# Optimization experiments

Hardware: AMD Instinct MI355X
Metric: run time of the kernel (lower is better)

The kernel has to match this reference:

```python
import jax, jax.numpy as jnp
from jax import lax
import numpy as np

NB_HEAD = 8
D_MODEL = 64
KERNEL = 3


def setup_inputs() -> dict:
    key = jax.random.key(0)
    k1, k2, k3, k4, k5 = jax.random.split(key, 5)
    B, N, T, D = 16, 1024, 24, D_MODEL
    value = jax.random.normal(k1, (B, N, T, D), dtype=jnp.float32)
    # Conv2d(d_model, d_model, (1, kernel_size)) weights (OIHW) + bias
    fan_in = D * 1 * KERNEL
    bound = 1.0 / np.sqrt(fan_in)
    W_conv = jax.random.uniform(k2, (D, D, 1, KERNEL), jnp.float32, -bound, bound)
    b_conv = jax.random.uniform(k3, (D,), jnp.float32, -bound, bound)
    # Linear(d_model, d_model): W (out, in), bias (out,)
    lb = 1.0 / np.sqrt(D)
    W_lin = jax.random.uniform(k4, (D, D), jnp.float32, -lb, lb)
    b_lin = jax.random.uniform(k5, (D,), jnp.float32, -lb, lb)
    return {"value": value, "W_conv": W_conv, "b_conv": b_conv,
            "W_lin": W_lin, "b_lin": b_lin}


def reference(value, W_conv, b_conv, W_lin, b_lin):
    B, N, T, D = value.shape
    h = NB_HEAD
    d_k = D // h
    pad = (KERNEL - 1) // 2
    # conv1D_aware_temporal_context1 on value.permute(0,3,1,2): (B, D, N, T)
    x = jnp.transpose(value, (0, 3, 1, 2))
    x = lax.conv_general_dilated(
        x, W_conv, window_strides=(1, 1), padding=[(0, 0), (pad, pad)],
        dimension_numbers=("NCHW", "OIHW", "NCHW"))
    x = x + b_conv[None, :, None, None]
    # view(B, h, d_k, N, T).permute(0,3,1,4,2) -> (B, N, h, T, d_k)
    v = jnp.transpose(x.reshape(B, h, d_k, N, T), (0, 3, 1, 4, 2))
    # relation_matrix_h is the tridiagonal all-ones band -> out[t] = v[t-1]+v[t]+v[t+1]
    vp = jnp.pad(v, ((0, 0), (0, 0), (0, 0), (1, 1), (0, 0)))
    v = vp[..., :-2, :] + vp[..., 1:-1, :] + vp[..., 2:, :]
    # transpose(2,3) then merge heads: (B, N, T, h*d_k)
    v = jnp.transpose(v, (0, 1, 3, 2, 4)).reshape(B, N, T, h * d_k)
    # linear_output1 + relu
    out = jax.nn.relu(jnp.einsum("bntd,od->bnto", v, W_lin) + b_lin)
    return out
```

## Files before the change

kernel.cpp:

```cpp
#include <hip/hip_runtime.h>
#include <hip/hip_bf16.h>


typedef __attribute__((ext_vector_type(8))) short short8;
typedef __attribute__((ext_vector_type(8))) __bf16 bf16x8;
typedef __attribute__((ext_vector_type(4))) float f4;

#define R_ROWS 8
#define VP_STRIDE 72
#define V_ROW_ELEMS (26 * VP_STRIDE)

__device__ __forceinline__ unsigned short f2bfu(float f) {
    return __bfloat16_as_ushort(__float2bfloat16(f));
}

__global__ void prep_kernel(const float* __restrict__ Wconv,
                            const float* __restrict__ bconv,
                            const float* __restrict__ Wlin,
                            const float* __restrict__ blin,
                            __hip_bfloat16* __restrict__ wbig,
                            float* __restrict__ biasC,
                            float* __restrict__ blinF) {
    __shared__ float Wl[4096];
    const int tid = threadIdx.x;
    for (int c = tid; c < 4096; c += 256) Wl[c] = Wlin[c];
    __syncthreads();
    int idx = blockIdx.x * 256 + tid;
    if (idx < 64 * 192) {
        int o = idx / 192;
        int j = idx - o * 192;
        int k = j >> 6;
        int i = j & 63;
        float acc = 0.0f;
        for (int c = 0; c < 64; ++c)
            acc += Wl[o * 64 + c] * Wconv[c * 192 + i * 3 + k];
        wbig[o * 192 + j] = __float2bfloat16(acc);
    } else if (idx < 64 * 192 + 64) {
        int o = idx - 64 * 192;
        float acc = 0.0f;
        for (int c = 0; c < 64; ++c)
            acc += Wl[o * 64 + c] * bconv[c];
        biasC[o] = acc;
    } else if (idx < 64 * 192 + 128) {
        int o = idx - (64 * 192 + 64);
        blinF[o] = blin[o];
    }
}

__global__ __launch_bounds__(256, 4) void fused_kernel(
    const float* __restrict__ value,
    const __hip_bfloat16* __restrict__ wbig,
    const float* __restrict__ biasC,
    const float* __restrict__ blinF,
    float* __restrict__ out) {
    __shared__ __align__(16) short Vlds[R_ROWS * V_ROW_ELEMS];

    const int tid = threadIdx.x;
    const int wave = tid >> 6;
    const int lane = tid & 63;
    const int lane15 = lane & 15;
    const int quad = lane >> 4;
    const long base_row = (long)blockIdx.x * R_ROWS;

    for (int c4 = tid; c4 < 3072; c4 += 256) {
        int r = c4 / 384;
        int rem = c4 - r * 384;
        int t = rem >> 4;
        int d4 = (rem & 15) << 2;
        f4 v = *(const f4*)(value + (base_row + r) * 1536 + t * 64 + d4);
        ushort4 u;
        u.x = f2bfu(v.x); u.y = f2bfu(v.y); u.z = f2bfu(v.z); u.w = f2bfu(v.w);
        *(ushort4*)(Vlds + r * V_ROW_ELEMS + (t + 1) * VP_STRIDE + d4) = u;
    }
    if (tid < 128) {
        int r = tid >> 4;
        int which = (tid >> 3) & 1;
        int d8 = (tid & 7) << 3;
        uint4 z; z.x = 0; z.y = 0; z.z = 0; z.w = 0;
        *(uint4*)(Vlds + r * V_ROW_ELEMS + which * (25 * VP_STRIDE) + d8) = z;
    }
    __syncthreads();

    f4 acc[3][4];
    #pragma unroll
    for (int a = 0; a < 3; ++a)
        #pragma unroll
        for (int b = 0; b < 4; ++b) {
            f4 zz = {0.f, 0.f, 0.f, 0.f};
            acc[a][b] = zz;
        }

    const int mt0 = wave * 3;
    int aoff[3];
    #pragma unroll
    for (int mt = 0; mt < 3; ++mt) {
        int m = (mt0 + mt) * 16 + lane15;
        int r = m / 24;
        int s = m - r * 24;
        aoff[mt] = r * V_ROW_ELEMS + s * VP_STRIDE;
    }
    const short* wsrc = (const short*)wbig;
    const int k0 = quad * 8;
    #pragma unroll
    for (int ks = 0; ks < 6; ++ks) {
        int k = ks * 32 + k0;
        int ka = ((k >> 6) * VP_STRIDE) + (k & 63);
        bf16x8 bfr[4], afr[3];
        #pragma unroll
        for (int nt = 0; nt < 4; ++nt)
            bfr[nt] = __builtin_bit_cast(bf16x8,
                *(const short8*)(wsrc + (nt * 16 + lane15) * 192 + k));
        #pragma unroll
        for (int mt = 0; mt < 3; ++mt)
            afr[mt] = __builtin_bit_cast(bf16x8,
                *(const short8*)(Vlds + aoff[mt] + ka));
        #pragma unroll
        for (int mt = 0; mt < 3; ++mt)
            #pragma unroll
            for (int nt = 0; nt < 4; ++nt)
                acc[mt][nt] = __builtin_amdgcn_mfma_f32_16x16x32_bf16(
                    afr[mt], bfr[nt], acc[mt][nt], 0, 0, 0);
    }

    float b3[4], b2[4];
    #pragma unroll
    for (int nt = 0; nt < 4; ++nt) {
        int o = nt * 16 + lane15;
        float bc = biasC[o];
        float bl = blinF[o];
        b3[nt] = 3.0f * bc + bl;
        b2[nt] = 2.0f * bc + bl;
    }
    const int srcP = (lane + 48) & 63;
    const int srcN = (lane + 16) & 63;
    #pragma unroll
    for (int mt = 0; mt < 3; ++mt) {
        const int mtp = (mt > 0) ? mt - 1 : 0;
        const int mtn = (mt < 2) ? mt + 1 : 2;
        #pragma unroll
        for (int nt = 0; nt < 4; ++nt) {
            float pin = __shfl(acc[mt][nt][3], srcP, 64);
            float pxr = __shfl(acc[mtp][nt][3], srcP, 64);
            float nin = __shfl(acc[mt][nt][0], srcN, 64);
            float nxr = __shfl(acc[mtn][nt][0], srcN, 64);
            float prev0 = (quad == 0) ? pxr : pin;
            float next3 = (quad == 3) ? nxr : nin;
            #pragma unroll
            for (int i = 0; i < 4; ++i) {
                int tq = mt * 16 + quad * 4 + i;
                int rr = (tq >= 24) ? 1 : 0;
                int t = tq - rr * 24;
                float s = acc[mt][nt][i];
                float prev = (i > 0) ? acc[mt][nt][i - 1] : prev0;
                float next = (i < 3) ? acc[mt][nt][i + 1] : next3;
                if (t > 0)  s += prev;
                if (t < 23) s += next;
                float bias = (t == 0 || t == 23) ? b2[nt] : b3[nt];
                float r = fmaxf(s + bias, 0.0f);
                long addr = ((base_row + 2 * wave + rr) * 24 + t) * 64
                            + nt * 16 + lane15;
                out[addr] = r;
            }
        }
    }
}

extern "C" void kernel_launch(void* const* d_in, const int* in_sizes, int n_in,
                              void* d_out, int out_size, void* d_ws, size_t ws_size,
                              hipStream_t stream) {
    const float* value = (const float*)d_in[0];
    const float* Wconv = (const float*)d_in[1];
    const float* bconv = (const float*)d_in[2];
    const float* Wlin  = (const float*)d_in[3];
    const float* blin  = (const float*)d_in[4];
    float* out = (float*)d_out;

    __hip_bfloat16* wbig = (__hip_bfloat16*)d_ws;
    float* biasC = (float*)((char*)d_ws + 24576);
    float* blinF = (float*)((char*)d_ws + 24832);

    prep_kernel<<<49, 256, 0, stream>>>(Wconv, bconv, Wlin, blin, wbig, biasC, blinF);
    fused_kernel<<<2048, 256, 0, stream>>>(value, wbig, biasC, blinF, out);
}
```

Baseline: 209.1 us.

## Persist blocks over four row groups with double-buffered LDS prefetch

Each block now processes four 8-row groups instead of one. The next group's global loads are issued into registers before the current group's MFMA work, then written to a second LDS buffer afterwards. Work is also split so each wave owns one 16-column output slice across all 12 M tiles, with its weight fragments held in registers for the whole kernel. The aim is to overlap memory loads with compute and cut repeated weight loads and block launch overhead. In exchange it doubles LDS use, raises register pressure, lowers occupancy (launch bounds 4 to 2), and launches only 512 blocks.

```diff
diff --git a/kernel.cpp b/kernel.cpp
--- a/kernel.cpp
+++ b/kernel.cpp
@@ -7,6 +7,7 @@
 typedef __attribute__((ext_vector_type(4))) float f4;
 
 #define R_ROWS 8
+#define GROUPS 4
 #define VP_STRIDE 72
 #define V_ROW_ELEMS (26 * VP_STRIDE)
 
@@ -47,121 +48,149 @@
     }
 }
 
-__global__ __launch_bounds__(256, 4) void fused_kernel(
+__global__ __launch_bounds__(256, 2) void fused_kernel(
     const float* __restrict__ value,
     const __hip_bfloat16* __restrict__ wbig,
     const float* __restrict__ biasC,
     const float* __restrict__ blinF,
     float* __restrict__ out) {
-    __shared__ __align__(16) short Vlds[R_ROWS * V_ROW_ELEMS];
+    __shared__ __align__(16) short Vlds[2][R_ROWS * V_ROW_ELEMS];
 
     const int tid = threadIdx.x;
     const int wave = tid >> 6;
     const int lane = tid & 63;
     const int lane15 = lane & 15;
     const int quad = lane >> 4;
-    const long base_row = (long)blockIdx.x * R_ROWS;
-
-    for (int c4 = tid; c4 < 3072; c4 += 256) {
+    const long block_row0 = (long)blockIdx.x * (R_ROWS * GROUPS);
+
+    int goff[12], loff[12];
+    #pragma unroll
+    for (int j = 0; j < 12; ++j) {
+        int c4 = tid + 256 * j;
         int r = c4 / 384;
         int rem = c4 - r * 384;
         int t = rem >> 4;
         int d4 = (rem & 15) << 2;
-        f4 v = *(const f4*)(value + (base_row + r) * 1536 + t * 64 + d4);
-        ushort4 u;
-        u.x = f2bfu(v.x); u.y = f2bfu(v.y); u.z = f2bfu(v.z); u.w = f2bfu(v.w);
-        *(ushort4*)(Vlds + r * V_ROW_ELEMS + (t + 1) * VP_STRIDE + d4) = u;
+        goff[j] = r * 1536 + t * 64 + d4;
+        loff[j] = r * V_ROW_ELEMS + (t + 1) * VP_STRIDE + d4;
     }
     if (tid < 128) {
         int r = tid >> 4;
         int which = (tid >> 3) & 1;
         int d8 = (tid & 7) << 3;
         uint4 z; z.x = 0; z.y = 0; z.z = 0; z.w = 0;
-        *(uint4*)(Vlds + r * V_ROW_ELEMS + which * (25 * VP_STRIDE) + d8) = z;
+        *(uint4*)(&Vlds[0][0] + r * V_ROW_ELEMS + which * (25 * VP_STRIDE) + d8) = z;
+        *(uint4*)(&Vlds[1][0] + r * V_ROW_ELEMS + which * (25 * VP_STRIDE) + d8) = z;
+    }
+
+    const short* wsrc = (const short*)wbig;
+    const int k0 = quad * 8;
+    bf16x8 breg[6];
+    #pragma unroll
+    for (int ks = 0; ks < 6; ++ks)
+        breg[ks] = __builtin_bit_cast(bf16x8,
+            *(const short8*)(wsrc + (wave * 16 + lane15) * 192 + ks * 32 + k0));
+
+    f4 pre[12];
+    {
+        const float* vb = value + block_row0 * 1536;
+        #pragma unroll
+        for (int j = 0; j < 12; ++j)
+            pre[j] = *(const f4*)(vb + goff[j]);
+        #pragma unroll
+        for (int j = 0; j < 12; ++j) {
+            ushort4 u;
+            u.x = f2bfu(pre[j].x); u.y = f2bfu(pre[j].y);
+            u.z = f2bfu(pre[j].z); u.w = f2bfu(pre[j].w);
+            *(ushort4*)(&Vlds[0][0] + loff[j]) = u;
+        }
     }
     __syncthreads();
 
-    f4 acc[3][4];
+    int aoff[12];
     #pragma unroll
-    for (int a = 0; a < 3; ++a)
-        #pragma unroll
-        for (int b = 0; b < 4; ++b) {
-            f4 zz = {0.f, 0.f, 0.f, 0.f};
-            acc[a][b] = zz;
-        }
-
-    const int mt0 = wave * 3;
-    int aoff[3];
-    #pragma unroll
-    for (int mt = 0; mt < 3; ++mt) {
-        int m = (mt0 + mt) * 16 + lane15;
+    for (int mt = 0; mt < 12; ++mt) {
+        int m = mt * 16 + lane15;
         int r = m / 24;
         int s = m - r * 24;
         aoff[mt] = r * V_ROW_ELEMS + s * VP_STRIDE;
     }
-    const short* wsrc = (const short*)wbig;
-    const int k0 = quad * 8;
-    #pragma unroll
-    for (int ks = 0; ks < 6; ++ks) {
-        int k = ks * 32 + k0;
-        int ka = ((k >> 6) * VP_STRIDE) + (k & 63);
-        bf16x8 bfr[4], afr[3];
-        #pragma unroll
-        for (int nt = 0; nt < 4; ++nt)
-            bfr[nt] = __builtin_bit_cast(bf16x8,
-                *(const short8*)(wsrc + (nt * 16 + lane15) * 192 + k));
-        #pragma unroll
-        for (int mt = 0; mt < 3; ++mt)
-            afr[mt] = __builtin_bit_cast(bf16x8,
-                *(const short8*)(Vlds + aoff[mt] + ka));
-        #pragma unroll
-        for (int mt = 0; mt < 3; ++mt)
-            #pragma unroll
-            for (int nt = 0; nt < 4; ++nt)
-                acc[mt][nt] = __builtin_amdgcn_mfma_f32_16x16x32_bf16(
-                    afr[mt], bfr[nt], acc[mt][nt], 0, 0, 0);
-    }
-
-    float b3[4], b2[4];
-    #pragma unroll
-    for (int nt = 0; nt < 4; ++nt) {
-        int o = nt * 16 + lane15;
-        float bc = biasC[o];
-        float bl = blinF[o];
-        b3[nt] = 3.0f * bc + bl;
-        b2[nt] = 2.0f * bc + bl;
-    }
+
+    const int o = wave * 16 + lane15;
+    const float bc = biasC[o];
+    const float bl = blinF[o];
+    const float b3 = 3.0f * bc + bl;
+    const float b2 = 2.0f * bc + bl;
     const int srcP = (lane + 48) & 63;
     const int srcN = (lane + 16) & 63;
-    #pragma unroll
-    for (int mt = 0; mt < 3; ++mt) {
-        const int mtp = (mt > 0) ? mt - 1 : 0;
-        const int mtn = (mt < 2) ? mt + 1 : 2;
-        #pragma unroll
-        for (int nt = 0; nt < 4; ++nt) {
-            float pin = __shfl(acc[mt][nt][3], srcP, 64);
-            float pxr = __shfl(acc[mtp][nt][3], srcP, 64);
-            float nin = __shfl(acc[mt][nt][0], srcN, 64);
-            float nxr = __shfl(acc[mtn][nt][0], srcN, 64);
+
+    int p = 0;
+    for (int g = 0; g < GROUPS; ++g) {
+        if (g + 1 < GROUPS) {
+            const float* vb = value + (block_row0 + (long)(g + 1) * R_ROWS) * 1536;
+            #pragma unroll
+            for (int j = 0; j < 12; ++j)
+                pre[j] = *(const f4*)(vb + goff[j]);
+        }
+
+        const short* Vcur = &Vlds[p][0];
+        f4 acc[12];
+        #pragma unroll
+        for (int mt = 0; mt < 12; ++mt) {
+            f4 zz = {0.f, 0.f, 0.f, 0.f};
+            acc[mt] = zz;
+        }
+        #pragma unroll
+        for (int ks = 0; ks < 6; ++ks) {
+            int k = ks * 32 + k0;
+            int ka = ((k >> 6) * VP_STRIDE) + (k & 63);
+            #pragma unroll
+            for (int mt = 0; mt < 12; ++mt) {
+                bf16x8 a = __builtin_bit_cast(bf16x8,
+                    *(const short8*)(Vcur + aoff[mt] + ka));
+                acc[mt] = __builtin_amdgcn_mfma_f32_16x16x32_bf16(
+                    a, breg[ks], acc[mt], 0, 0, 0);
+            }
+        }
+
+        const long grow0 = block_row0 + (long)g * R_ROWS;
+        #pragma unroll
+        for (int mt = 0; mt < 12; ++mt) {
+            const int mtp = (mt > 0) ? mt - 1 : 0;
+            const int mtn = (mt < 11) ? mt + 1 : 11;
+            float pin = __shfl(acc[mt][3], srcP, 64);
+            float pxr = __shfl(acc[mtp][3], srcP, 64);
+            float nin = __shfl(acc[mt][0], srcN, 64);
+            float nxr = __shfl(acc[mtn][0], srcN, 64);
             float prev0 = (quad == 0) ? pxr : pin;
             float next3 = (quad == 3) ? nxr : nin;
             #pragma unroll
             for (int i = 0; i < 4; ++i) {
-                int tq = mt * 16 + quad * 4 + i;
-                int rr = (tq >= 24) ? 1 : 0;
-                int t = tq - rr * 24;
-                float s = acc[mt][nt][i];
-                float prev = (i > 0) ? acc[mt][nt][i - 1] : prev0;
-                float next = (i < 3) ? acc[mt][nt][i + 1] : next3;
+                int rowq = mt * 16 + quad * 4 + i;
+                int rr = rowq / 24;
+                int t = rowq - rr * 24;
+                float s = acc[mt][i];
+                float prev = (i > 0) ? acc[mt][i - 1] : prev0;
+                float next = (i < 3) ? acc[mt][i + 1] : next3;
                 if (t > 0)  s += prev;
                 if (t < 23) s += next;
-                float bias = (t == 0 || t == 23) ? b2[nt] : b3[nt];
-                float r = fmaxf(s + bias, 0.0f);
-                long addr = ((base_row + 2 * wave + rr) * 24 + t) * 64
-                            + nt * 16 + lane15;
-                out[addr] = r;
+                float r = fmaxf(s + ((t == 0 || t == 23) ? b2 : b3), 0.0f);
+                out[((grow0 + rr) * 24 + t) * 64 + o] = r;
             }
         }
+
+        if (g + 1 < GROUPS) {
+            short* Vnxt = &Vlds[p ^ 1][0];
+            #pragma unroll
+            for (int j = 0; j < 12; ++j) {
+                ushort4 u;
+                u.x = f2bfu(pre[j].x); u.y = f2bfu(pre[j].y);
+                u.z = f2bfu(pre[j].z); u.w = f2bfu(pre[j].w);
+                *(ushort4*)(Vnxt + loff[j]) = u;
+            }
+            __syncthreads();
+        }
+        p ^= 1;
     }
 }
 
@@ -180,5 +209,5 @@
     float* blinF = (float*)((char*)d_ws + 24832);
 
     prep_kernel<<<49, 256, 0, stream>>>(Wconv, bconv, Wlin, blin, wbig, biasC, blinF);
-    fused_kernel<<<2048, 256, 0, stream>>>(value, wbig, biasC, blinF, out);
-}
+    fused_kernel<<<512, 256, 0, stream>>>(value, wbig, biasC, blinF, out);
+}
```

Result: faster. 200.1 us (-4.3%).

## Drop LDS staging; load value directly into MFMA B-fragments per wave row

Applied to the files above, without the earlier changes.

Each wave now handles one (b,n) row and reads its fp32 activations straight from global memory into bf16 MFMA operands, replacing the LDS staging buffer and the block-wide barrier. The GEMM is transposed so weights form the A operand and time steps the columns, with 2 time tiles padded to 32 (8 wasted lanes). The temporal neighbour sum uses ds_bpermute within quads, and the grid doubles to 4096 blocks. This removes LDS traffic and synchronisation, at the cost of redundant overlapping global loads (each value row is reread for three time shifts) and padded MFMA work.

```diff
diff --git a/kernel.cpp b/kernel.cpp
--- a/kernel.cpp
+++ b/kernel.cpp
@@ -5,14 +5,6 @@
 typedef __attribute__((ext_vector_type(8))) short short8;
 typedef __attribute__((ext_vector_type(8))) __bf16 bf16x8;
 typedef __attribute__((ext_vector_type(4))) float f4;
-
-#define R_ROWS 8
-#define VP_STRIDE 72
-#define V_ROW_ELEMS (26 * VP_STRIDE)
-
-__device__ __forceinline__ unsigned short f2bfu(float f) {
-    return __bfloat16_as_ushort(__float2bfloat16(f));
-}
 
 __global__ void prep_kernel(const float* __restrict__ Wconv,
                             const float* __restrict__ bconv,
@@ -47,119 +39,103 @@
     }
 }
 
+__device__ __forceinline__ float bperm(int idx, float v) {
+    return __int_as_float(__builtin_amdgcn_ds_bpermute(idx, __float_as_int(v)));
+}
+
 __global__ __launch_bounds__(256, 4) void fused_kernel(
     const float* __restrict__ value,
     const __hip_bfloat16* __restrict__ wbig,
     const float* __restrict__ biasC,
     const float* __restrict__ blinF,
     float* __restrict__ out) {
-    __shared__ __align__(16) short Vlds[R_ROWS * V_ROW_ELEMS];
-
     const int tid = threadIdx.x;
-    const int wave = tid >> 6;
     const int lane = tid & 63;
     const int lane15 = lane & 15;
     const int quad = lane >> 4;
-    const long base_row = (long)blockIdx.x * R_ROWS;
+    const long row = (long)blockIdx.x * 4 + (tid >> 6);
+    const float* vrow = value + row * 1536;
 
-    for (int c4 = tid; c4 < 3072; c4 += 256) {
-        int r = c4 / 384;
-        int rem = c4 - r * 384;
-        int t = rem >> 4;
-        int d4 = (rem & 15) << 2;
-        f4 v = *(const f4*)(value + (base_row + r) * 1536 + t * 64 + d4);
-        ushort4 u;
-        u.x = f2bfu(v.x); u.y = f2bfu(v.y); u.z = f2bfu(v.z); u.w = f2bfu(v.w);
-        *(ushort4*)(Vlds + r * V_ROW_ELEMS + (t + 1) * VP_STRIDE + d4) = u;
-    }
-    if (tid < 128) {
-        int r = tid >> 4;
-        int which = (tid >> 3) & 1;
-        int d8 = (tid & 7) << 3;
-        uint4 z; z.x = 0; z.y = 0; z.z = 0; z.w = 0;
-        *(uint4*)(Vlds + r * V_ROW_ELEMS + which * (25 * VP_STRIDE) + d8) = z;
-    }
-    __syncthreads();
-
-    f4 acc[3][4];
+    f4 acc[2][4];
     #pragma unroll
-    for (int a = 0; a < 3; ++a)
+    for (int nt = 0; nt < 2; ++nt)
         #pragma unroll
-        for (int b = 0; b < 4; ++b) {
+        for (int mt = 0; mt < 4; ++mt) {
             f4 zz = {0.f, 0.f, 0.f, 0.f};
-            acc[a][b] = zz;
+            acc[nt][mt] = zz;
         }
 
-    const int mt0 = wave * 3;
-    int aoff[3];
-    #pragma unroll
-    for (int mt = 0; mt < 3; ++mt) {
-        int m = (mt0 + mt) * 16 + lane15;
-        int r = m / 24;
-        int s = m - r * 24;
-        aoff[mt] = r * V_ROW_ELEMS + s * VP_STRIDE;
-    }
     const short* wsrc = (const short*)wbig;
-    const int k0 = quad * 8;
+    const int wko = lane15 * 192 + quad * 8;
+    const short8 z8 = {0, 0, 0, 0, 0, 0, 0, 0};
+
     #pragma unroll
     for (int ks = 0; ks < 6; ++ks) {
-        int k = ks * 32 + k0;
-        int ka = ((k >> 6) * VP_STRIDE) + (k & 63);
-        bf16x8 bfr[4], afr[3];
+        bf16x8 wf[4];
         #pragma unroll
-        for (int nt = 0; nt < 4; ++nt)
-            bfr[nt] = __builtin_bit_cast(bf16x8,
-                *(const short8*)(wsrc + (nt * 16 + lane15) * 192 + k));
+        for (int mt = 0; mt < 4; ++mt)
+            wf[mt] = __builtin_bit_cast(bf16x8,
+                *(const short8*)(wsrc + mt * 16 * 192 + wko + ks * 32));
+        const int tau = ks >> 1;
+        const int i0 = (ks & 1) * 32 + quad * 8;
         #pragma unroll
-        for (int mt = 0; mt < 3; ++mt)
-            afr[mt] = __builtin_bit_cast(bf16x8,
-                *(const short8*)(Vlds + aoff[mt] + ka));
-        #pragma unroll
-        for (int mt = 0; mt < 3; ++mt)
+        for (int nt = 0; nt < 2; ++nt) {
+            int m = nt * 16 + lane15;
+            int st = m + tau - 1;
+            bool valid = (st >= 0) && (st < 24);
+            int stc = st < 0 ? 0 : (st > 23 ? 23 : st);
+            const float* src = vrow + stc * 64 + i0;
+            f4 lo = *(const f4*)(src);
+            f4 hi = *(const f4*)(src + 4);
+            short8 vs;
+            vs[0] = (short)__bfloat16_as_ushort(__float2bfloat16(lo.x));
+            vs[1] = (short)__bfloat16_as_ushort(__float2bfloat16(lo.y));
+            vs[2] = (short)__bfloat16_as_ushort(__float2bfloat16(lo.z));
+            vs[3] = (short)__bfloat16_as_ushort(__float2bfloat16(lo.w));
+            vs[4] = (short)__bfloat16_as_ushort(__float2bfloat16(hi.x));
+            vs[5] = (short)__bfloat16_as_ushort(__float2bfloat16(hi.y));
+            vs[6] = (short)__bfloat16_as_ushort(__float2bfloat16(hi.z));
+            vs[7] = (short)__bfloat16_as_ushort(__float2bfloat16(hi.w));
+            vs = valid ? vs : z8;
+            bf16x8 vfrag = __builtin_bit_cast(bf16x8, vs);
             #pragma unroll
-            for (int nt = 0; nt < 4; ++nt)
-                acc[mt][nt] = __builtin_amdgcn_mfma_f32_16x16x32_bf16(
-                    afr[mt], bfr[nt], acc[mt][nt], 0, 0, 0);
+            for (int mt = 0; mt < 4; ++mt)
+                acc[nt][mt] = __builtin_amdgcn_mfma_f32_16x16x32_bf16(
+                    wf[mt], vfrag, acc[nt][mt], 0, 0, 0);
+        }
     }
 
-    float b3[4], b2[4];
+    const int idxP = ((quad << 4) | ((lane15 + 15) & 15)) << 2;
+    const int idxN = ((quad << 4) | ((lane15 + 1) & 15)) << 2;
+    const bool sel15 = (lane15 == 15);
+    const bool sel0 = (lane15 == 0);
+    const bool valid_m1 = (lane15 < 8);
+
     #pragma unroll
-    for (int nt = 0; nt < 4; ++nt) {
-        int o = nt * 16 + lane15;
-        float bc = biasC[o];
-        float bl = blinF[o];
-        b3[nt] = 3.0f * bc + bl;
-        b2[nt] = 2.0f * bc + bl;
-    }
-    const int srcP = (lane + 48) & 63;
-    const int srcN = (lane + 16) & 63;
-    #pragma unroll
-    for (int mt = 0; mt < 3; ++mt) {
-        const int mtp = (mt > 0) ? mt - 1 : 0;
-        const int mtn = (mt < 2) ? mt + 1 : 2;
+    for (int mt = 0; mt < 4; ++mt) {
+        f4 bc = *(const f4*)(biasC + mt * 16 + quad * 4);
+        f4 bl = *(const f4*)(blinF + mt * 16 + quad * 4);
         #pragma unroll
-        for (int nt = 0; nt < 4; ++nt) {
-            float pin = __shfl(acc[mt][nt][3], srcP, 64);
-            float pxr = __shfl(acc[mtp][nt][3], srcP, 64);
-            float nin = __shfl(acc[mt][nt][0], srcN, 64);
-            float nxr = __shfl(acc[mtn][nt][0], srcN, 64);
-            float prev0 = (quad == 0) ? pxr : pin;
-            float next3 = (quad == 3) ? nxr : nin;
+        for (int nt = 0; nt < 2; ++nt) {
+            const int m = nt * 16 + lane15;
+            const bool has_prev = (nt == 1) || (lane15 != 0);
+            const bool has_next = (nt == 0) || (lane15 != 7);
+            const bool edge = (nt == 0) ? sel0 : (lane15 == 7);
+            const bool do_store = (nt == 0) || valid_m1;
+            long obase = row * 1536 + m * 64 + mt * 16 + quad * 4;
             #pragma unroll
             for (int i = 0; i < 4; ++i) {
-                int tq = mt * 16 + quad * 4 + i;
-                int rr = (tq >= 24) ? 1 : 0;
-                int t = tq - rr * 24;
-                float s = acc[mt][nt][i];
-                float prev = (i > 0) ? acc[mt][nt][i - 1] : prev0;
-                float next = (i < 3) ? acc[mt][nt][i + 1] : next3;
-                if (t > 0)  s += prev;
-                if (t < 23) s += next;
-                float bias = (t == 0 || t == 23) ? b2[nt] : b3[nt];
+                float zc = acc[nt][mt][i];
+                float xp = (nt == 1 && sel15) ? acc[0][mt][i] : acc[nt][mt][i];
+                float xn = (nt == 0 && sel0) ? acc[1][mt][i] : acc[nt][mt][i];
+                float prev = bperm(idxP, xp);
+                float next = bperm(idxN, xn);
+                float s = zc;
+                if (has_prev) s += prev;
+                if (has_next) s += next;
+                float bias = (edge ? 2.0f : 3.0f) * bc[i] + bl[i];
                 float r = fmaxf(s + bias, 0.0f);
-                long addr = ((base_row + 2 * wave + rr) * 24 + t) * 64
-                            + nt * 16 + lane15;
-                out[addr] = r;
+                if (do_store) out[obase + i] = r;
             }
         }
     }
@@ -180,5 +156,5 @@
     float* blinF = (float*)((char*)d_ws + 24832);
 
     prep_kernel<<<49, 256, 0, stream>>>(Wconv, bconv, Wlin, blin, wbig, biasC, blinF);
-    fused_kernel<<<2048, 256, 0, stream>>>(value, wbig, biasC, blinF, out);
+    fused_kernel<<<4096, 256, 0, stream>>>(value, wbig, biasC, blinF, out);
 }
```

New measurement: 252.5 us. 20.8% more time.
